# Optimization experiments

Measured on AMD Instinct MI355X. Metric: run time of the kernel, lower is better.

Reference implementation:

```python
import jax, jax.numpy as jnp
import numpy as np

KS = 3        # kernel_size == stride (non-overlapping patches)
ALPHA = 0.1


def setup_inputs() -> dict:
    key = jax.random.key(0)
    k1, k2, k3 = jax.random.split(key, 3)
    b, c, m, n = 32, 256, 56, 56
    l = (m - KS) // KS + 1   # 18
    kk = (n - KS) // KS + 1  # 18
    activation = jax.random.normal(k1, (b, c, m, n), dtype=jnp.float32)
    # precomputed bernoulli(0.5) draws (0/1), kept as int so they are constants
    rc = jax.random.randint(k2, (b, c, m, n), 0, 2, dtype=jnp.int32)
    p_patch_mask = jax.random.randint(k3, (b, c, l, kk), 0, 2, dtype=jnp.int32)
    return {"activation": activation, "rc": rc, "p_patch_mask": p_patch_mask}


def reference(activation, rc, p_patch_mask):
    b, c, m, n = activation.shape
    l, k = p_patch_mask.shape[2], p_patch_mask.shape[3]
    dt = activation.dtype

    # per-(b,c) spatial peak -> [b,c,1,1]
    peak = jnp.max(activation, axis=(2, 3), keepdims=True)
    pc = (activation == peak).astype(dt)          # peak indicator
    bc_dash = rc.astype(dt) * pc                  # rc * pc (peak dropout mask)

    # broadcast patch-level bernoulli mask to pixel level over covered region
    full = jnp.repeat(jnp.repeat(p_patch_mask.astype(dt), KS, axis=2), KS, axis=3)
    # uncovered border (fold leaves it zero) -> pad with zeros to (m, n)
    full = jnp.pad(full, ((0, 0), (0, 0), (0, m - l * KS), (0, n - k * KS)))
    # zero-out patch mask at peak locations (bc_dd_batch[activation==peak]=0)
    bc_dd = full * (1.0 - pc)

    bc = bc_dash + bc_dd
    return jnp.where(bc >= 1.0, activation * ALPHA, activation)
```

## Files before the change

kernel.cpp:

```cpp
#include <hip/hip_runtime.h>
#include <math.h>

#define KS     3
#define ALPHA  0.1f
#define M      56
#define N      56
#define L      18
#define KK     18
#define PIX    (M * N)
#define VEC    (PIX / 4)
#define WAVES  4
#define NTHR   (WAVES * 64)
#define COVER  (L * KS)

typedef float vf4 __attribute__((ext_vector_type(4)));

__device__ __forceinline__ float rmax4(vf4 x) {
    return fmaxf(fmaxf(x.x, x.y), fmaxf(x.z, x.w));
}

__device__ __forceinline__ vf4 proc4(vf4 x, int v, float peak, size_t base,
                                     const int* __restrict__ rc,
                                     const int* sm) {
    const int p0 = v * 4;
    const int i  = v / 14;
    const int j0 = p0 - i * N;
    const bool inrow = (i < COVER);
    const int  mrow  = (i / 3) * KK;

    vf4 o;
#pragma unroll
    for (int e = 0; e < 4; ++e) {
        const float a = x[e];
        const int   j = j0 + e;
        bool cond;
        if (a == peak) {
            cond = (rc[base + (size_t)(p0 + e)] != 0);
        } else {
            cond = inrow && (j < COVER) && (sm[mrow + j / 3] != 0);
        }
        o[e] = cond ? a * ALPHA : a;
    }
    return o;
}

__global__ __launch_bounds__(NTHR) void div_block_kernel(
    const float* __restrict__ act,
    const int*   __restrict__ rc,
    const int*   __restrict__ pmask,
    float*       __restrict__ out,
    int planes) {

    const int tid = threadIdx.x;
    const int w   = tid >> 6;
    const int l   = tid & 63;
    const int plane = blockIdx.x * WAVES + w;
    if (plane >= planes) return;

    const size_t base = (size_t)plane * PIX;
    const vf4* a4 = (const vf4*)(act + base);
    vf4*       o4 = (vf4*)(out + base);

    __shared__ int smask[WAVES][L * KK];
    int* sm = smask[w];
    for (int s = l; s < L * KK; s += 64)
        sm[s] = pmask[(size_t)plane * (L * KK) + s];

    vf4 x0  = a4[l];
    vf4 x1  = a4[l + 1 * 64];
    vf4 x2  = a4[l + 2 * 64];
    vf4 x3  = a4[l + 3 * 64];
    vf4 x4  = a4[l + 4 * 64];
    vf4 x5  = a4[l + 5 * 64];
    vf4 x6  = a4[l + 6 * 64];
    vf4 x7  = a4[l + 7 * 64];
    vf4 x8  = a4[l + 8 * 64];
    vf4 x9  = a4[l + 9 * 64];
    vf4 x10 = a4[l + 10 * 64];
    vf4 x11 = a4[l + 11 * 64];
    const bool has12 = (l < (VEC - 12 * 64));
    vf4 x12;
    if (has12) x12 = a4[l + 12 * 64];
    else       x12 = (vf4){-INFINITY, -INFINITY, -INFINITY, -INFINITY};

    float m0 = fmaxf(rmax4(x0),  rmax4(x1));
    float m1 = fmaxf(rmax4(x2),  rmax4(x3));
    float m2 = fmaxf(rmax4(x4),  rmax4(x5));
    float m3 = fmaxf(rmax4(x6),  rmax4(x7));
    float m4 = fmaxf(rmax4(x8),  rmax4(x9));
    float m5 = fmaxf(rmax4(x10), rmax4(x11));
    float mx = fmaxf(fmaxf(fmaxf(m0, m1), fmaxf(m2, m3)),
                     fmaxf(fmaxf(m4, m5), rmax4(x12)));
#pragma unroll
    for (int off = 32; off > 0; off >>= 1)
        mx = fmaxf(mx, __shfl_xor(mx, off, 64));
    const float peak = mx;

    __builtin_nontemporal_store(proc4(x0,  l,           peak, base, rc, sm), &o4[l]);
    __builtin_nontemporal_store(proc4(x1,  l + 1 * 64,  peak, base, rc, sm), &o4[l + 1 * 64]);
    __builtin_nontemporal_store(proc4(x2,  l + 2 * 64,  peak, base, rc, sm), &o4[l + 2 * 64]);
    __builtin_nontemporal_store(proc4(x3,  l + 3 * 64,  peak, base, rc, sm), &o4[l + 3 * 64]);
    __builtin_nontemporal_store(proc4(x4,  l + 4 * 64,  peak, base, rc, sm), &o4[l + 4 * 64]);
    __builtin_nontemporal_store(proc4(x5,  l + 5 * 64,  peak, base, rc, sm), &o4[l + 5 * 64]);
    __builtin_nontemporal_store(proc4(x6,  l + 6 * 64,  peak, base, rc, sm), &o4[l + 6 * 64]);
    __builtin_nontemporal_store(proc4(x7,  l + 7 * 64,  peak, base, rc, sm), &o4[l + 7 * 64]);
    __builtin_nontemporal_store(proc4(x8,  l + 8 * 64,  peak, base, rc, sm), &o4[l + 8 * 64]);
    __builtin_nontemporal_store(proc4(x9,  l + 9 * 64,  peak, base, rc, sm), &o4[l + 9 * 64]);
    __builtin_nontemporal_store(proc4(x10, l + 10 * 64, peak, base, rc, sm), &o4[l + 10 * 64]);
    __builtin_nontemporal_store(proc4(x11, l + 11 * 64, peak, base, rc, sm), &o4[l + 11 * 64]);
    if (has12)
        __builtin_nontemporal_store(proc4(x12, l + 12 * 64, peak, base, rc, sm), &o4[l + 12 * 64]);
}

extern "C" void kernel_launch(void* const* d_in, const int* in_sizes, int n_in,
                              void* d_out, int out_size, void* d_ws, size_t ws_size,
                              hipStream_t stream) {
    const float* act   = (const float*)d_in[0];
    const int*   rc    = (const int*)d_in[1];
    const int*   pmask = (const int*)d_in[2];
    float*       out   = (float*)d_out;

    const int planes = in_sizes[0] / PIX;
    const int blocks = (planes + WAVES - 1) / WAVES;
    div_block_kernel<<<blocks, NTHR, 0, stream>>>(act, rc, pmask, out, planes);
}
```

Measured before the change: 41.65 us.

## Stream stores before peak reduction and patch up peak pixels afterward

The kernel now writes each chunk's output using only the patch mask as soon as it is loaded, instead of holding all thirteen vectors in registers until the plane peak is known. Only lanes whose local max equals the peak reload their data and overwrite the peak pixels using rc. Each shared-memory mask lookup is also reduced to two loads per vec4. This lowers register pressure and lets stores overlap loads. The cost is re-reading activations on peak lanes and relying on a waitcnt to order the corrected store after the earlier nontemporal store.

```diff
diff --git a/kernel.cpp b/kernel.cpp
--- a/kernel.cpp
+++ b/kernel.cpp
@@ -12,36 +12,12 @@
 #define WAVES  4
 #define NTHR   (WAVES * 64)
 #define COVER  (L * KS)
+#define CHUNKS 13
 
 typedef float vf4 __attribute__((ext_vector_type(4)));
 
 __device__ __forceinline__ float rmax4(vf4 x) {
     return fmaxf(fmaxf(x.x, x.y), fmaxf(x.z, x.w));
-}
-
-__device__ __forceinline__ vf4 proc4(vf4 x, int v, float peak, size_t base,
-                                     const int* __restrict__ rc,
-                                     const int* sm) {
-    const int p0 = v * 4;
-    const int i  = v / 14;
-    const int j0 = p0 - i * N;
-    const bool inrow = (i < COVER);
-    const int  mrow  = (i / 3) * KK;
-
-    vf4 o;
-#pragma unroll
-    for (int e = 0; e < 4; ++e) {
-        const float a = x[e];
-        const int   j = j0 + e;
-        bool cond;
-        if (a == peak) {
-            cond = (rc[base + (size_t)(p0 + e)] != 0);
-        } else {
-            cond = inrow && (j < COVER) && (sm[mrow + j / 3] != 0);
-        }
-        o[e] = cond ? a * ALPHA : a;
-    }
-    return o;
 }
 
 __global__ __launch_bounds__(NTHR) void div_block_kernel(
@@ -66,50 +42,57 @@
     for (int s = l; s < L * KK; s += 64)
         sm[s] = pmask[(size_t)plane * (L * KK) + s];
 
-    vf4 x0  = a4[l];
-    vf4 x1  = a4[l + 1 * 64];
-    vf4 x2  = a4[l + 2 * 64];
-    vf4 x3  = a4[l + 3 * 64];
-    vf4 x4  = a4[l + 4 * 64];
-    vf4 x5  = a4[l + 5 * 64];
-    vf4 x6  = a4[l + 6 * 64];
-    vf4 x7  = a4[l + 7 * 64];
-    vf4 x8  = a4[l + 8 * 64];
-    vf4 x9  = a4[l + 9 * 64];
-    vf4 x10 = a4[l + 10 * 64];
-    vf4 x11 = a4[l + 11 * 64];
-    const bool has12 = (l < (VEC - 12 * 64));
-    vf4 x12;
-    if (has12) x12 = a4[l + 12 * 64];
-    else       x12 = (vf4){-INFINITY, -INFINITY, -INFINITY, -INFINITY};
+    float lmax = -INFINITY;
+#pragma unroll
+    for (int c = 0; c < CHUNKS; ++c) {
+        const int v = l + c * 64;
+        if (v < VEC) {
+            vf4 x = a4[v];
+            lmax = fmaxf(lmax, rmax4(x));
 
-    float m0 = fmaxf(rmax4(x0),  rmax4(x1));
-    float m1 = fmaxf(rmax4(x2),  rmax4(x3));
-    float m2 = fmaxf(rmax4(x4),  rmax4(x5));
-    float m3 = fmaxf(rmax4(x6),  rmax4(x7));
-    float m4 = fmaxf(rmax4(x8),  rmax4(x9));
-    float m5 = fmaxf(rmax4(x10), rmax4(x11));
-    float mx = fmaxf(fmaxf(fmaxf(m0, m1), fmaxf(m2, m3)),
-                     fmaxf(fmaxf(m4, m5), rmax4(x12)));
+            const int i    = v / 14;
+            const int j0   = (v - i * 14) * 4;
+            const int mrow = (i < COVER ? (i / 3) : (L - 1)) * KK;
+            const int c0   = j0 / 3;
+            const int c1   = (j0 + 3) / 3;
+            const int ma   = sm[mrow + (c0 < KK ? c0 : KK - 1)];
+            const int mb   = sm[mrow + (c1 < KK ? c1 : KK - 1)];
+            const bool inrow = (i < COVER);
+
+            vf4 o;
+#pragma unroll
+            for (int e = 0; e < 4; ++e) {
+                const int j  = j0 + e;
+                const int mv = ((j / 3) == c0) ? ma : mb;
+                const bool cond = inrow && (j < COVER) && (mv != 0);
+                o[e] = cond ? x[e] * ALPHA : x[e];
+            }
+            __builtin_nontemporal_store(o, &o4[v]);
+        }
+    }
+
+    float peak = lmax;
 #pragma unroll
     for (int off = 32; off > 0; off >>= 1)
-        mx = fmaxf(mx, __shfl_xor(mx, off, 64));
-    const float peak = mx;
+        peak = fmaxf(peak, __shfl_xor(peak, off, 64));
 
-    __builtin_nontemporal_store(proc4(x0,  l,           peak, base, rc, sm), &o4[l]);
-    __builtin_nontemporal_store(proc4(x1,  l + 1 * 64,  peak, base, rc, sm), &o4[l + 1 * 64]);
-    __builtin_nontemporal_store(proc4(x2,  l + 2 * 64,  peak, base, rc, sm), &o4[l + 2 * 64]);
-    __builtin_nontemporal_store(proc4(x3,  l + 3 * 64,  peak, base, rc, sm), &o4[l + 3 * 64]);
-    __builtin_nontemporal_store(proc4(x4,  l + 4 * 64,  peak, base, rc, sm), &o4[l + 4 * 64]);
-    __builtin_nontemporal_store(proc4(x5,  l + 5 * 64,  peak, base, rc, sm), &o4[l + 5 * 64]);
-    __builtin_nontemporal_store(proc4(x6,  l + 6 * 64,  peak, base, rc, sm), &o4[l + 6 * 64]);
-    __builtin_nontemporal_store(proc4(x7,  l + 7 * 64,  peak, base, rc, sm), &o4[l + 7 * 64]);
-    __builtin_nontemporal_store(proc4(x8,  l + 8 * 64,  peak, base, rc, sm), &o4[l + 8 * 64]);
-    __builtin_nontemporal_store(proc4(x9,  l + 9 * 64,  peak, base, rc, sm), &o4[l + 9 * 64]);
-    __builtin_nontemporal_store(proc4(x10, l + 10 * 64, peak, base, rc, sm), &o4[l + 10 * 64]);
-    __builtin_nontemporal_store(proc4(x11, l + 11 * 64, peak, base, rc, sm), &o4[l + 11 * 64]);
-    if (has12)
-        __builtin_nontemporal_store(proc4(x12, l + 12 * 64, peak, base, rc, sm), &o4[l + 12 * 64]);
+    if (lmax == peak) {
+#pragma unroll
+        for (int c = 0; c < CHUNKS; ++c) {
+            const int v = l + c * 64;
+            if (v < VEC) {
+                vf4 x = a4[v];
+#pragma unroll
+                for (int e = 0; e < 4; ++e) {
+                    if (x[e] == peak) {
+                        asm volatile("s_waitcnt vmcnt(0)" ::: "memory");
+                        const size_t p = base + (size_t)(v * 4 + e);
+                        out[p] = (rc[p] != 0) ? x[e] * ALPHA : x[e];
+                    }
+                }
+            }
+        }
+    }
 }
 
 extern "C" void kernel_launch(void* const* d_in, const int* in_sizes, int n_in,
```

New measurement: 41.59 us. No clear change (-0.1%).
